# Kernel optimization log

Hardware: AMD Instinct MI355X
Metric: run time of the kernel (lower is better)

Reference implementation:

```python
import jax, jax.numpy as jnp
import numpy as np

NUM_QUERIES, NUM_KEYS = 32, 64
QUERY_DIM, KEY_DIM = 512, 512
NUM_HEADS, ATTN_DIM = 8, 64
EMBED_DIM = NUM_HEADS * ATTN_DIM  # 512
OUT_DIM = 512
TEMPERATURE = float(np.sqrt(ATTN_DIM))


def setup_inputs() -> dict:
    key = jax.random.key(0)
    ks = jax.random.split(key, 6)
    b = 1.0 / TEMPERATURE
    b_p = 1.0 / float(np.sqrt(OUT_DIM))
    q = jax.random.normal(ks[0], (NUM_QUERIES, 2048, QUERY_DIM), dtype=jnp.float32)
    k = jax.random.normal(ks[1], (NUM_KEYS, 2048, KEY_DIM), dtype=jnp.float32)
    query_weight = jax.random.uniform(ks[2], (NUM_QUERIES, QUERY_DIM, EMBED_DIM), minval=-b, maxval=b, dtype=jnp.float32)
    key_weight = jax.random.uniform(ks[3], (NUM_KEYS, KEY_DIM, EMBED_DIM), minval=-b, maxval=b, dtype=jnp.float32)
    value_weight = jax.random.uniform(ks[4], (NUM_KEYS, KEY_DIM, EMBED_DIM), minval=-b, maxval=b, dtype=jnp.float32)
    proj_weight = jax.random.uniform(ks[5], (NUM_QUERIES, EMBED_DIM, OUT_DIM), minval=-b_p, maxval=b_p, dtype=jnp.float32)
    return {"q": q, "k": k, "query_weight": query_weight, "key_weight": key_weight,
            "value_weight": value_weight, "proj_weight": proj_weight}


def reference(q, k, query_weight, key_weight, value_weight, proj_weight):
    Qn, bs, _ = q.shape
    Kn = k.shape[0]
    H, D = NUM_HEADS, ATTN_DIM
    # per-slot projections: (slots, bs, embed) -> split embed into heads
    query = jnp.einsum('ibq,iqe->ibe', q, query_weight).reshape(Qn, bs, H, D)
    key_e = jnp.einsum('jbk,jke->jbe', k, key_weight).reshape(Kn, bs, H, D)
    value = jnp.einsum('jbk,jke->jbe', k, value_weight).reshape(Kn, bs, H, D)
    # logits over key slots per (batch, head, query slot)
    logits = jnp.einsum('ibhd,jbhd->bhij', query, key_e) / TEMPERATURE
    attn = jax.nn.softmax(logits, axis=-1)  # softmax over key slots
    out = jnp.einsum('bhij,jbhd->ibhd', attn, value).reshape(Qn, bs, H * D)
    out = jnp.einsum('ibe,ieo->ibo', out, proj_weight)
    return out
```

## Files before the change

kernel.cpp:

```cpp
#include <hip/hip_runtime.h>

typedef __attribute__((ext_vector_type(8))) short bf16x8;
typedef __attribute__((ext_vector_type(4))) float f32x4;
typedef __attribute__((ext_vector_type(4))) unsigned short us4;

__device__ __forceinline__ unsigned short f2bf(float f) {
    unsigned u = __builtin_bit_cast(unsigned, f);
    u += 0x7FFFu + ((u >> 16) & 1u);
    return (unsigned short)(u >> 16);
}

__device__ __forceinline__ void gl_lds16(const void* g, void* l) {
    __builtin_amdgcn_global_load_lds(
        (const __attribute__((address_space(1))) unsigned int*)g,
        (__attribute__((address_space(3))) unsigned int*)l, 16, 0, 0);
}

__global__ __launch_bounds__(256) void cast_f32_bf16(const float* __restrict__ in,
                                                     unsigned short* __restrict__ out, int n4) {
    int i = blockIdx.x * blockDim.x + threadIdx.x;
    int stride = gridDim.x * blockDim.x;
    for (; i < n4; i += stride) {
        float4 v = ((const float4*)in)[i];
        us4 o;
        o.x = f2bf(v.x); o.y = f2bf(v.y); o.z = f2bf(v.z); o.w = f2bf(v.w);
        ((us4*)out)[i] = o;
    }
}

__global__ __launch_bounds__(256) void transpose_w(const float* __restrict__ wq,
                                                   const float* __restrict__ wk,
                                                   const float* __restrict__ wv,
                                                   const float* __restrict__ wp,
                                                   unsigned short* __restrict__ Wt) {
    int sb = blockIdx.x >> 6;
    int tile = blockIdx.x & 63;
    const float* src;
    if (sb < 32)       src = wq + (size_t)sb * 262144;
    else if (sb < 96)  src = wk + (size_t)(sb - 32) * 262144;
    else if (sb < 160) src = wv + (size_t)(sb - 96) * 262144;
    else               src = wp + (size_t)(sb - 160) * 262144;
    unsigned short* dst = Wt + (size_t)sb * 262144;
    int q0 = (tile & 7) * 64, e0 = (tile >> 3) * 64;
    __shared__ float t[64][65];
    int tx = threadIdx.x & 63, ty = threadIdx.x >> 6;
    for (int i = 0; i < 16; i++) {
        int r = ty + 4 * i;
        t[r][tx] = src[(size_t)(q0 + r) * 512 + e0 + tx];
    }
    __syncthreads();
    int tx2 = threadIdx.x & 31, ty2 = threadIdx.x >> 5;
    for (int i = 0; i < 8; i++) {
        int e = ty2 + 8 * i;
        int qq = tx2 * 2;
        unsigned a = f2bf(t[qq][e]);
        unsigned bb = f2bf(t[qq + 1][e]);
        *(unsigned*)&dst[(size_t)(e0 + e) * 512 + q0 + qq] = a | (bb << 16);
    }
}

__global__ __launch_bounds__(256, 2) void gemm_qkv(const unsigned short* __restrict__ qb,
                                                   const unsigned short* __restrict__ kb,
                                                   const unsigned short* __restrict__ Wt,
                                                   unsigned short* __restrict__ Qs,
                                                   unsigned short* __restrict__ Ks,
                                                   unsigned short* __restrict__ Vs) {
    __shared__ __align__(16) unsigned short lds[2][2][8192];
    int s = blockIdx.y;
    const unsigned short* A;
    unsigned short* Cw;
    if (s < 32)      { A = qb + (size_t)s * 1048576;        Cw = Qs + (size_t)s * 1048576; }
    else if (s < 96) { A = kb + (size_t)(s - 32) * 1048576; Cw = Ks + (size_t)(s - 32) * 1048576; }
    else             { A = kb + (size_t)(s - 96) * 1048576; Cw = Vs + (size_t)(s - 96) * 1048576; }
    const unsigned short* B = Wt + (size_t)s * 262144;
    int tm = blockIdx.x >> 2, tn = blockIdx.x & 3;
    int l = threadIdx.x & 63, w = threadIdx.x >> 6;
    const unsigned short* Ag = A + (size_t)(tm * 128) * 512;
    const unsigned short* Bg = B + (size_t)(tn * 128) * 512;
    int wr = (w >> 1) * 64, wc = (w & 1) * 64;
    int srcs = ((l & 7) ^ (l >> 3)) * 8;

    f32x4 acc[4][4] = {};

#define STAGE(bufi, k0)                                                            \
    for (int p = 0; p < 4; p++) {                                                  \
        int row = w * 32 + p * 8 + (l >> 3);                                       \
        gl_lds16(Ag + (size_t)row * 512 + (k0) + srcs, &lds[bufi][0][(w*32+p*8)*64]); \
        gl_lds16(Bg + (size_t)row * 512 + (k0) + srcs, &lds[bufi][1][(w*32+p*8)*64]); \
    }

    STAGE(0, 0)
    __syncthreads();
    for (int t = 0; t < 8; t++) {
        int cur = t & 1;
        if (t < 7) { STAGE(cur ^ 1, (t + 1) * 64) }
        bf16x8 aF[2][4], bF[2][4];
        for (int kc = 0; kc < 2; kc++) {
            int sp = ((kc * 4 + (l >> 4)) ^ (l & 7)) * 8;
            for (int m = 0; m < 4; m++)
                aF[kc][m] = *(const bf16x8*)&lds[cur][0][(wr + m * 16 + (l & 15)) * 64 + sp];
            for (int n = 0; n < 4; n++)
                bF[kc][n] = *(const bf16x8*)&lds[cur][1][(wc + n * 16 + (l & 15)) * 64 + sp];
        }
        for (int kc = 0; kc < 2; kc++)
            for (int m = 0; m < 4; m++)
                for (int n = 0; n < 4; n++)
                    acc[m][n] = __builtin_amdgcn_mfma_f32_16x16x32_bf16(aF[kc][m], bF[kc][n], acc[m][n], 0, 0, 0);
        __syncthreads();
    }
#undef STAGE

    unsigned short* Cs = &lds[0][0][0];
    for (int m = 0; m < 4; m++)
        for (int n = 0; n < 4; n++)
            for (int r = 0; r < 4; r++)
                Cs[(wr + m * 16 + (l >> 4) * 4 + r) * 136 + wc + n * 16 + (l & 15)] = f2bf(acc[m][n][r]);
    __syncthreads();
    for (int rnd = 0; rnd < 8; rnd++) {
        int row = rnd * 16 + (threadIdx.x >> 4);
        int c8 = (threadIdx.x & 15) * 8;
        bf16x8 v = *(const bf16x8*)&Cs[row * 136 + c8];
        *(bf16x8*)&Cw[(size_t)(tm * 128 + row) * 512 + tn * 128 + c8] = v;
    }
}

__global__ __launch_bounds__(256, 2) void gemm_proj(const unsigned short* __restrict__ Ain,
                                                    const unsigned short* __restrict__ Wt,
                                                    float* __restrict__ out) {
    __shared__ __align__(16) unsigned short lds[2][2][8192];
    int s = blockIdx.y;
    const unsigned short* A = Ain + (size_t)s * 1048576;
    const unsigned short* B = Wt + (size_t)(160 + s) * 262144;
    int tm = blockIdx.x >> 2, tn = blockIdx.x & 3;
    int l = threadIdx.x & 63, w = threadIdx.x >> 6;
    const unsigned short* Ag = A + (size_t)(tm * 128) * 512;
    const unsigned short* Bg = B + (size_t)(tn * 128) * 512;
    int wr = (w >> 1) * 64, wc = (w & 1) * 64;
    int srcs = ((l & 7) ^ (l >> 3)) * 8;

    f32x4 acc[4][4] = {};

#define STAGE(bufi, k0)                                                            \
    for (int p = 0; p < 4; p++) {                                                  \
        int row = w * 32 + p * 8 + (l >> 3);                                       \
        gl_lds16(Ag + (size_t)row * 512 + (k0) + srcs, &lds[bufi][0][(w*32+p*8)*64]); \
        gl_lds16(Bg + (size_t)row * 512 + (k0) + srcs, &lds[bufi][1][(w*32+p*8)*64]); \
    }

    STAGE(0, 0)
    __syncthreads();
    for (int t = 0; t < 8; t++) {
        int cur = t & 1;
        if (t < 7) { STAGE(cur ^ 1, (t + 1) * 64) }
        bf16x8 aF[2][4], bF[2][4];
        for (int kc = 0; kc < 2; kc++) {
            int sp = ((kc * 4 + (l >> 4)) ^ (l & 7)) * 8;
            for (int m = 0; m < 4; m++)
                aF[kc][m] = *(const bf16x8*)&lds[cur][0][(wr + m * 16 + (l & 15)) * 64 + sp];
            for (int n = 0; n < 4; n++)
                bF[kc][n] = *(const bf16x8*)&lds[cur][1][(wc + n * 16 + (l & 15)) * 64 + sp];
        }
        for (int kc = 0; kc < 2; kc++)
            for (int m = 0; m < 4; m++)
                for (int n = 0; n < 4; n++)
                    acc[m][n] = __builtin_amdgcn_mfma_f32_16x16x32_bf16(aF[kc][m], bF[kc][n], acc[m][n], 0, 0, 0);
        __syncthreads();
    }
#undef STAGE

    float* Cf = (float*)&lds[0][0][0];
    for (int pass = 0; pass < 2; pass++) {
        if (wr == pass * 64) {
            for (int m = 0; m < 4; m++)
                for (int n = 0; n < 4; n++)
                    for (int r = 0; r < 4; r++)
                        Cf[(m * 16 + (l >> 4) * 4 + r) * 132 + wc + n * 16 + (l & 15)] = acc[m][n][r];
        }
        __syncthreads();
        for (int rnd = 0; rnd < 8; rnd++) {
            int row = rnd * 8 + (threadIdx.x >> 5);
            int c4 = (threadIdx.x & 31) * 4;
            float4 v = *(const float4*)&Cf[row * 132 + c4];
            *(float4*)&out[(size_t)s * 1048576 + (size_t)(tm * 128 + pass * 64 + row) * 512 + tn * 128 + c4] = v;
        }
        __syncthreads();
    }
}

__global__ __launch_bounds__(256) void attn_k(const unsigned short* __restrict__ Qs,
                                              const unsigned short* __restrict__ Ks,
                                              const unsigned short* __restrict__ Vs,
                                              unsigned short* __restrict__ Aout) {
    __shared__ __align__(16) unsigned short pl[4][32 * 72];
    __shared__ __align__(16) unsigned short vt[4][64 * 88];
    const size_t SL = 1048576;
    int w = threadIdx.x >> 6, l = threadIdx.x & 63;
    int g = blockIdx.x * 4 + w;
    int b = g >> 3, h = g & 7;
    const unsigned short* Qp = Qs + (size_t)b * 512 + h * 64;
    const unsigned short* Kp = Ks + (size_t)b * 512 + h * 64;
    const unsigned short* Vp = Vs + (size_t)b * 512 + h * 64;
    int lr = l & 15, lc = l >> 4;
    unsigned short* vtw = vt[w];

    for (int jr = 0; jr < 64; jr += 8) {
        int j = jr + (l >> 3), d0 = (l & 7) * 8;
        bf16x8 v = *(const bf16x8*)&Vp[(size_t)j * SL + d0];
        for (int e = 0; e < 8; e++) vtw[(d0 + e) * 88 + j] = (unsigned short)v[e];
    }

    bf16x8 aQ[2][2], bK[4][2];
    for (int m = 0; m < 2; m++)
        for (int kc = 0; kc < 2; kc++)
            aQ[m][kc] = *(const bf16x8*)&Qp[(size_t)(m * 16 + lr) * SL + kc * 32 + lc * 8];
    for (int n = 0; n < 4; n++)
        for (int kc = 0; kc < 2; kc++)
            bK[n][kc] = *(const bf16x8*)&Kp[(size_t)(n * 16 + lr) * SL + kc * 32 + lc * 8];

    f32x4 acc[2][4] = {};
    for (int kc = 0; kc < 2; kc++)
        for (int m = 0; m < 2; m++)
            for (int n = 0; n < 4; n++)
                acc[m][n] = __builtin_amdgcn_mfma_f32_16x16x32_bf16(aQ[m][kc], bK[n][kc], acc[m][n], 0, 0, 0);

    const float sc = 0.18033688011112042f;
    for (int m = 0; m < 2; m++) {
        for (int r = 0; r < 4; r++) {
            float v = acc[m][0][r];
            for (int n = 1; n < 4; n++) v = fmaxf(v, acc[m][n][r]);
            for (int sh = 1; sh < 16; sh <<= 1) v = fmaxf(v, __shfl_xor(v, sh));
            float ssum = 0.f;
            for (int n = 0; n < 4; n++) {
                float p = exp2f((acc[m][n][r] - v) * sc);
                acc[m][n][r] = p;
                ssum += p;
            }
            for (int sh = 1; sh < 16; sh <<= 1) ssum += __shfl_xor(ssum, sh);
            float inv = 1.0f / ssum;
            for (int n = 0; n < 4; n++)
                pl[w][(m * 16 + lc * 4 + r) * 72 + n * 16 + lr] = f2bf(acc[m][n][r] * inv);
        }
    }

    bf16x8 aP[2][2], bV[4][2];
    for (int m = 0; m < 2; m++)
        for (int kc = 0; kc < 2; kc++)
            aP[m][kc] = *(const bf16x8*)&pl[w][(m * 16 + lr) * 72 + kc * 32 + lc * 8];
    for (int n = 0; n < 4; n++)
        for (int kc = 0; kc < 2; kc++)
            bV[n][kc] = *(const bf16x8*)&vtw[(n * 16 + lr) * 88 + kc * 32 + lc * 8];

    f32x4 o[2][4] = {};
    for (int kc = 0; kc < 2; kc++)
        for (int m = 0; m < 2; m++)
            for (int n = 0; n < 4; n++)
                o[m][n] = __builtin_amdgcn_mfma_f32_16x16x32_bf16(aP[m][kc], bV[n][kc], o[m][n], 0, 0, 0);

    for (int m = 0; m < 2; m++)
        for (int n = 0; n < 4; n++)
            for (int r = 0; r < 4; r++)
                vtw[(m * 16 + lc * 4 + r) * 88 + n * 16 + lr] = f2bf(o[m][n][r]);
    for (int rnd = 0; rnd < 4; rnd++) {
        int i = rnd * 8 + (l >> 3), d0 = (l & 7) * 8;
        bf16x8 v = *(const bf16x8*)&vtw[i * 88 + d0];
        *(bf16x8*)&Aout[(size_t)i * SL + (size_t)b * 512 + h * 64 + d0] = v;
    }
}

extern "C" void kernel_launch(void* const* d_in, const int* in_sizes, int n_in,
                              void* d_out, int out_size, void* d_ws, size_t ws_size,
                              hipStream_t stream) {
    const float* q  = (const float*)d_in[0];
    const float* k  = (const float*)d_in[1];
    const float* wq = (const float*)d_in[2];
    const float* wk = (const float*)d_in[3];
    const float* wv = (const float*)d_in[4];
    const float* wp = (const float*)d_in[5];

    char* ws = (char*)d_ws;
    unsigned short* qb = (unsigned short*)(ws);
    unsigned short* kb = (unsigned short*)(ws + ((size_t)64 << 20));
    unsigned short* Wt = (unsigned short*)(ws + ((size_t)192 << 20));
    unsigned short* Qs = (unsigned short*)(ws + ((size_t)288 << 20));
    unsigned short* Ks = (unsigned short*)(ws + ((size_t)352 << 20));
    unsigned short* Vs = (unsigned short*)(ws + ((size_t)480 << 20));
    unsigned short* Aout = qb;
    float* out = (float*)d_out;

    hipLaunchKernelGGL(cast_f32_bf16, dim3(2048), dim3(256), 0, stream, q, qb, 32 * 2048 * 512 / 4);
    hipLaunchKernelGGL(cast_f32_bf16, dim3(2048), dim3(256), 0, stream, k, kb, 64 * 2048 * 512 / 4);
    hipLaunchKernelGGL(transpose_w, dim3(192 * 64), dim3(256), 0, stream, wq, wk, wv, wp, Wt);
    hipLaunchKernelGGL(gemm_qkv, dim3(64, 160), dim3(256), 0, stream, qb, kb, Wt, Qs, Ks, Vs);
    hipLaunchKernelGGL(attn_k, dim3(4096), dim3(256), 0, stream, Qs, Ks, Vs, Aout);
    hipLaunchKernelGGL(gemm_proj, dim3(64, 32), dim3(256), 0, stream, Aout, Wt, out);
}
```

Baseline: 613.8 us.

## Deepen GEMM pipeline to four LDS stages with XCD-aware block remapping

Both GEMM kernels move from a double-buffered LDS pipeline to a 4-buffer ring that prefetches three k-tiles ahead. Full __syncthreads are replaced with vmcnt-based partial waits plus raw barriers, and MFMA sections are wrapped in s_setprio. The grid is flattened to 1D and remapped so consecutive blocks on each XCD share A tiles, with K and V projections of the same key slot interleaved for L2 reuse. The 64KB LDS buffer drops occupancy to one block per CU, which the deeper prefetch must make up for.

```diff
diff --git a/kernel.cpp b/kernel.cpp
--- a/kernel.cpp
+++ b/kernel.cpp
@@ -59,21 +59,29 @@
     }
 }
 
-__global__ __launch_bounds__(256, 2) void gemm_qkv(const unsigned short* __restrict__ qb,
+__global__ __launch_bounds__(256, 1) void gemm_qkv(const unsigned short* __restrict__ qb,
                                                    const unsigned short* __restrict__ kb,
                                                    const unsigned short* __restrict__ Wt,
                                                    unsigned short* __restrict__ Qs,
                                                    unsigned short* __restrict__ Ks,
                                                    unsigned short* __restrict__ Vs) {
-    __shared__ __align__(16) unsigned short lds[2][2][8192];
-    int s = blockIdx.y;
+    __shared__ __align__(16) unsigned short lds[4][2][8192];
+    int bid = blockIdx.x;
+    int logical = (bid & 7) * 1280 + (bid >> 3);
+    int sIdx = logical >> 6, x = logical & 63;
+    int tm = x >> 2, tn = x & 3;
     const unsigned short* A;
     unsigned short* Cw;
-    if (s < 32)      { A = qb + (size_t)s * 1048576;        Cw = Qs + (size_t)s * 1048576; }
-    else if (s < 96) { A = kb + (size_t)(s - 32) * 1048576; Cw = Ks + (size_t)(s - 32) * 1048576; }
-    else             { A = kb + (size_t)(s - 96) * 1048576; Cw = Vs + (size_t)(s - 96) * 1048576; }
-    const unsigned short* B = Wt + (size_t)s * 262144;
-    int tm = blockIdx.x >> 2, tn = blockIdx.x & 3;
+    int wslot;
+    if (sIdx < 32) {
+        A = qb + (size_t)sIdx * 1048576; Cw = Qs + (size_t)sIdx * 1048576; wslot = sIdx;
+    } else {
+        int p = sIdx - 32, ks = p >> 1;
+        A = kb + (size_t)ks * 1048576;
+        if (p & 1) { Cw = Vs + (size_t)ks * 1048576; wslot = 96 + ks; }
+        else       { Cw = Ks + (size_t)ks * 1048576; wslot = 32 + ks; }
+    }
+    const unsigned short* B = Wt + (size_t)wslot * 262144;
     int l = threadIdx.x & 63, w = threadIdx.x >> 6;
     const unsigned short* Ag = A + (size_t)(tm * 128) * 512;
     const unsigned short* Bg = B + (size_t)(tn * 128) * 512;
@@ -82,34 +90,44 @@
 
     f32x4 acc[4][4] = {};
 
-#define STAGE(bufi, k0)                                                            \
-    for (int p = 0; p < 4; p++) {                                                  \
-        int row = w * 32 + p * 8 + (l >> 3);                                       \
+#define STAGE(bufi, k0)                                                               \
+    for (int p = 0; p < 4; p++) {                                                     \
+        int row = w * 32 + p * 8 + (l >> 3);                                          \
         gl_lds16(Ag + (size_t)row * 512 + (k0) + srcs, &lds[bufi][0][(w*32+p*8)*64]); \
         gl_lds16(Bg + (size_t)row * 512 + (k0) + srcs, &lds[bufi][1][(w*32+p*8)*64]); \
     }
 
-    STAGE(0, 0)
-    __syncthreads();
+    STAGE(0, 0) STAGE(1, 64) STAGE(2, 128)
+    asm volatile("s_waitcnt vmcnt(16)" ::: "memory");
+    __builtin_amdgcn_s_barrier();
+
+#pragma unroll
     for (int t = 0; t < 8; t++) {
-        int cur = t & 1;
-        if (t < 7) { STAGE(cur ^ 1, (t + 1) * 64) }
+        if (t <= 4) { STAGE((t + 3) & 3, (t + 3) * 64) }
+        const unsigned short* la = &lds[t & 3][0][0];
+        const unsigned short* lb = &lds[t & 3][1][0];
         bf16x8 aF[2][4], bF[2][4];
         for (int kc = 0; kc < 2; kc++) {
             int sp = ((kc * 4 + (l >> 4)) ^ (l & 7)) * 8;
             for (int m = 0; m < 4; m++)
-                aF[kc][m] = *(const bf16x8*)&lds[cur][0][(wr + m * 16 + (l & 15)) * 64 + sp];
-            for (int n = 0; n < 4; n++)
-                bF[kc][n] = *(const bf16x8*)&lds[cur][1][(wc + n * 16 + (l & 15)) * 64 + sp];
-        }
+                aF[kc][m] = *(const bf16x8*)&la[(wr + m * 16 + (l & 15)) * 64 + sp];
+            for (int n = 0; n < 4; n++)
+                bF[kc][n] = *(const bf16x8*)&lb[(wc + n * 16 + (l & 15)) * 64 + sp];
+        }
+        __builtin_amdgcn_s_setprio(1);
         for (int kc = 0; kc < 2; kc++)
             for (int m = 0; m < 4; m++)
                 for (int n = 0; n < 4; n++)
                     acc[m][n] = __builtin_amdgcn_mfma_f32_16x16x32_bf16(aF[kc][m], bF[kc][n], acc[m][n], 0, 0, 0);
-        __syncthreads();
+        __builtin_amdgcn_s_setprio(0);
+        if (t <= 4)      asm volatile("s_waitcnt vmcnt(16)" ::: "memory");
+        else if (t == 5) asm volatile("s_waitcnt vmcnt(8)" ::: "memory");
+        else if (t == 6) asm volatile("s_waitcnt vmcnt(0)" ::: "memory");
+        if (t < 7) __builtin_amdgcn_s_barrier();
     }
 #undef STAGE
 
+    __syncthreads();
     unsigned short* Cs = &lds[0][0][0];
     for (int m = 0; m < 4; m++)
         for (int n = 0; n < 4; n++)
@@ -124,14 +142,16 @@
     }
 }
 
-__global__ __launch_bounds__(256, 2) void gemm_proj(const unsigned short* __restrict__ Ain,
+__global__ __launch_bounds__(256, 1) void gemm_proj(const unsigned short* __restrict__ Ain,
                                                     const unsigned short* __restrict__ Wt,
                                                     float* __restrict__ out) {
-    __shared__ __align__(16) unsigned short lds[2][2][8192];
-    int s = blockIdx.y;
+    __shared__ __align__(16) unsigned short lds[4][2][8192];
+    int bid = blockIdx.x;
+    int logical = (bid & 7) * 256 + (bid >> 3);
+    int s = logical >> 6, x = logical & 63;
+    int tm = x >> 2, tn = x & 3;
     const unsigned short* A = Ain + (size_t)s * 1048576;
     const unsigned short* B = Wt + (size_t)(160 + s) * 262144;
-    int tm = blockIdx.x >> 2, tn = blockIdx.x & 3;
     int l = threadIdx.x & 63, w = threadIdx.x >> 6;
     const unsigned short* Ag = A + (size_t)(tm * 128) * 512;
     const unsigned short* Bg = B + (size_t)(tn * 128) * 512;
@@ -140,34 +160,44 @@
 
     f32x4 acc[4][4] = {};
 
-#define STAGE(bufi, k0)                                                            \
-    for (int p = 0; p < 4; p++) {                                                  \
-        int row = w * 32 + p * 8 + (l >> 3);                                       \
+#define STAGE(bufi, k0)                                                               \
+    for (int p = 0; p < 4; p++) {                                                     \
+        int row = w * 32 + p * 8 + (l >> 3);                                          \
         gl_lds16(Ag + (size_t)row * 512 + (k0) + srcs, &lds[bufi][0][(w*32+p*8)*64]); \
         gl_lds16(Bg + (size_t)row * 512 + (k0) + srcs, &lds[bufi][1][(w*32+p*8)*64]); \
     }
 
-    STAGE(0, 0)
-    __syncthreads();
+    STAGE(0, 0) STAGE(1, 64) STAGE(2, 128)
+    asm volatile("s_waitcnt vmcnt(16)" ::: "memory");
+    __builtin_amdgcn_s_barrier();
+
+#pragma unroll
     for (int t = 0; t < 8; t++) {
-        int cur = t & 1;
-        if (t < 7) { STAGE(cur ^ 1, (t + 1) * 64) }
+        if (t <= 4) { STAGE((t + 3) & 3, (t + 3) * 64) }
+        const unsigned short* la = &lds[t & 3][0][0];
+        const unsigned short* lb = &lds[t & 3][1][0];
         bf16x8 aF[2][4], bF[2][4];
         for (int kc = 0; kc < 2; kc++) {
             int sp = ((kc * 4 + (l >> 4)) ^ (l & 7)) * 8;
             for (int m = 0; m < 4; m++)
-                aF[kc][m] = *(const bf16x8*)&lds[cur][0][(wr + m * 16 + (l & 15)) * 64 + sp];
-            for (int n = 0; n < 4; n++)
-                bF[kc][n] = *(const bf16x8*)&lds[cur][1][(wc + n * 16 + (l & 15)) * 64 + sp];
-        }
+                aF[kc][m] = *(const bf16x8*)&la[(wr + m * 16 + (l & 15)) * 64 + sp];
+            for (int n = 0; n < 4; n++)
+                bF[kc][n] = *(const bf16x8*)&lb[(wc + n * 16 + (l & 15)) * 64 + sp];
+        }
+        __builtin_amdgcn_s_setprio(1);
         for (int kc = 0; kc < 2; kc++)
             for (int m = 0; m < 4; m++)
                 for (int n = 0; n < 4; n++)
                     acc[m][n] = __builtin_amdgcn_mfma_f32_16x16x32_bf16(aF[kc][m], bF[kc][n], acc[m][n], 0, 0, 0);
-        __syncthreads();
+        __builtin_amdgcn_s_setprio(0);
+        if (t <= 4)      asm volatile("s_waitcnt vmcnt(16)" ::: "memory");
+        else if (t == 5) asm volatile("s_waitcnt vmcnt(8)" ::: "memory");
+        else if (t == 6) asm volatile("s_waitcnt vmcnt(0)" ::: "memory");
+        if (t < 7) __builtin_amdgcn_s_barrier();
     }
 #undef STAGE
 
+    __syncthreads();
     float* Cf = (float*)&lds[0][0][0];
     for (int pass = 0; pass < 2; pass++) {
         if (wr == pass * 64) {
@@ -290,7 +320,7 @@
     hipLaunchKernelGGL(cast_f32_bf16, dim3(2048), dim3(256), 0, stream, q, qb, 32 * 2048 * 512 / 4);
     hipLaunchKernelGGL(cast_f32_bf16, dim3(2048), dim3(256), 0, stream, k, kb, 64 * 2048 * 512 / 4);
     hipLaunchKernelGGL(transpose_w, dim3(192 * 64), dim3(256), 0, stream, wq, wk, wv, wp, Wt);
-    hipLaunchKernelGGL(gemm_qkv, dim3(64, 160), dim3(256), 0, stream, qb, kb, Wt, Qs, Ks, Vs);
+    hipLaunchKernelGGL(gemm_qkv, dim3(10240), dim3(256), 0, stream, qb, kb, Wt, Qs, Ks, Vs);
     hipLaunchKernelGGL(attn_k, dim3(4096), dim3(256), 0, stream, Qs, Ks, Vs, Aout);
-    hipLaunchKernelGGL(gemm_proj, dim3(64, 32), dim3(256), 0, stream, Aout, Wt, out);
-}
+    hipLaunchKernelGGL(gemm_proj, dim3(2048), dim3(256), 0, stream, Aout, Wt, out);
+}
```

After: 655.7 us. 6.8% more time.

## Use 256x256 tiles with 8 waves and ping-pong pipelined GEMM for projections

Applied to the files above, without the earlier changes.

Replaces the 128x128, 4-wave batched GEMMs for the QKV and output projections with a shared 256x256-tile routine run by 512 threads. The routine uses a fine-grained schedule that interleaves global-to-LDS staging with MFMA quarter blocks, separated by explicit barriers and vmcnt waits, and raises wave priority around the MFMAs. Block indices are remapped across XCDs so that K and V tiles sharing the same input slot run close together. The larger tiles cut operand re-reads from global memory and LDS per FLOP, at the cost of one block per CU, more registers and a more complex barrier schedule.

```diff
diff --git a/kernel.cpp b/kernel.cpp
--- a/kernel.cpp
+++ b/kernel.cpp
@@ -59,131 +59,182 @@
     }
 }
 
-__global__ __launch_bounds__(256, 2) void gemm_qkv(const unsigned short* __restrict__ qb,
+__device__ __forceinline__ void gemm256(const unsigned short* __restrict__ Ag,
+                                        const unsigned short* __restrict__ Bg,
+                                        unsigned short (&lds)[2][2][16384],
+                                        f32x4 (&acc)[8][4]) {
+    const int tid = threadIdx.x;
+    const int l = tid & 63, wid = tid >> 6;
+    const int wr = (wid >> 2) * 128, wc = (wid & 3) * 64;
+    const int lr = l & 15, shi = l >> 4;
+    const int srcs = ((l & 7) ^ ((l >> 3) & 7)) * 8;
+    const int grow = l >> 3;
+
+    bf16x8 af[4][2], bf[2][2][2];
+
+#define STG_(which, hh, t) do {                                                     \
+    const unsigned short* gp = (which) ? Bg : Ag;                                   \
+    _Pragma("unroll")                                                               \
+    for (int q = 0; q < 2; q++) {                                                   \
+        int lrow = (hh) * 128 + wid * 16 + q * 8;                                   \
+        gl_lds16(gp + (size_t)(lrow + grow) * 512 + (t) * 64 + srcs,                \
+                 &lds[(t) & 1][which][lrow * 64]);                                  \
+    } } while (0)
+
+#define LDA_(cur, mh) do {                                                          \
+    _Pragma("unroll") for (int m = 0; m < 4; m++)                                   \
+    _Pragma("unroll") for (int ks = 0; ks < 2; ks++)                                \
+        af[m][ks] = *(const bf16x8*)&lds[cur][0]                                    \
+            [(wr + (mh) * 64 + m * 16 + lr) * 64 + ((ks * 4 + shi) ^ (l & 7)) * 8]; \
+    } while (0)
+
+#define LDB_(cur, nh) do {                                                          \
+    _Pragma("unroll") for (int n = 0; n < 2; n++)                                   \
+    _Pragma("unroll") for (int ks = 0; ks < 2; ks++)                                \
+        bf[nh][n][ks] = *(const bf16x8*)&lds[cur][1]                                \
+            [(wc + (nh) * 32 + n * 16 + lr) * 64 + ((ks * 4 + shi) ^ (l & 7)) * 8]; \
+    } while (0)
+
+#define MM_(mh, nh) do {                                                            \
+    __builtin_amdgcn_s_setprio(1);                                                  \
+    _Pragma("unroll") for (int m = 0; m < 4; m++)                                   \
+    _Pragma("unroll") for (int n = 0; n < 2; n++)                                   \
+    _Pragma("unroll") for (int ks = 0; ks < 2; ks++)                                \
+        acc[(mh) * 4 + m][(nh) * 2 + n] = __builtin_amdgcn_mfma_f32_16x16x32_bf16(  \
+            af[m][ks], bf[nh][n][ks], acc[(mh) * 4 + m][(nh) * 2 + n], 0, 0, 0);    \
+    __builtin_amdgcn_s_setprio(0);                                                  \
+    } while (0)
+
+#define FENCE_ asm volatile("" ::: "memory")
+#define BAR_ do { FENCE_; __builtin_amdgcn_s_barrier(); FENCE_; } while (0)
+
+    STG_(0, 0, 0); STG_(0, 1, 0); STG_(1, 0, 0); STG_(1, 1, 0);
+    STG_(1, 0, 1); STG_(1, 1, 1);
+    asm volatile("s_waitcnt vmcnt(4)" ::: "memory");
+    BAR_;
+
+#pragma unroll
+    for (int i = 0; i < 4; i++) {
+        LDA_(0, 0); LDB_(0, 0);
+        STG_(0, 0, 2 * i + 1);
+        BAR_; MM_(0, 0); BAR_;
+        LDB_(0, 1);
+        STG_(0, 1, 2 * i + 1);
+        BAR_; MM_(0, 1); BAR_;
+        LDA_(0, 1);
+        if (i < 3) STG_(1, 0, 2 * i + 2);
+        BAR_; MM_(1, 0); BAR_;
+        if (i < 3) STG_(1, 1, 2 * i + 2);
+        BAR_; MM_(1, 1);
+        if (i < 3) asm volatile("s_waitcnt vmcnt(4)" ::: "memory");
+        else       asm volatile("s_waitcnt vmcnt(0)" ::: "memory");
+        BAR_;
+        LDA_(1, 0); LDB_(1, 0);
+        if (i < 3) STG_(0, 0, 2 * i + 2);
+        BAR_; MM_(0, 0); BAR_;
+        LDB_(1, 1);
+        if (i < 3) STG_(0, 1, 2 * i + 2);
+        BAR_; MM_(0, 1); BAR_;
+        LDA_(1, 1);
+        if (i <= 2) STG_(1, 0, 2 * i + 3);
+        BAR_; MM_(1, 0); BAR_;
+        if (i <= 2) STG_(1, 1, 2 * i + 3);
+        BAR_; MM_(1, 1);
+        if (i < 3) asm volatile("s_waitcnt vmcnt(4)" ::: "memory");
+        else       asm volatile("s_waitcnt vmcnt(0)" ::: "memory");
+        BAR_;
+    }
+#undef STG_
+#undef LDA_
+#undef LDB_
+#undef MM_
+}
+
+__global__ __launch_bounds__(512, 1) void gemm_qkv(const unsigned short* __restrict__ qb,
                                                    const unsigned short* __restrict__ kb,
                                                    const unsigned short* __restrict__ Wt,
                                                    unsigned short* __restrict__ Qs,
                                                    unsigned short* __restrict__ Ks,
                                                    unsigned short* __restrict__ Vs) {
-    __shared__ __align__(16) unsigned short lds[2][2][8192];
-    int s = blockIdx.y;
+    __shared__ __align__(16) unsigned short lds[2][2][16384];
+    int bid = blockIdx.x;
+    int logical = (bid & 7) * 320 + (bid >> 3);
+    int sIdx = logical >> 4, x = logical & 15;
+    int tm = x >> 1, tn = x & 1;
     const unsigned short* A;
     unsigned short* Cw;
-    if (s < 32)      { A = qb + (size_t)s * 1048576;        Cw = Qs + (size_t)s * 1048576; }
-    else if (s < 96) { A = kb + (size_t)(s - 32) * 1048576; Cw = Ks + (size_t)(s - 32) * 1048576; }
-    else             { A = kb + (size_t)(s - 96) * 1048576; Cw = Vs + (size_t)(s - 96) * 1048576; }
-    const unsigned short* B = Wt + (size_t)s * 262144;
-    int tm = blockIdx.x >> 2, tn = blockIdx.x & 3;
-    int l = threadIdx.x & 63, w = threadIdx.x >> 6;
-    const unsigned short* Ag = A + (size_t)(tm * 128) * 512;
-    const unsigned short* Bg = B + (size_t)(tn * 128) * 512;
-    int wr = (w >> 1) * 64, wc = (w & 1) * 64;
-    int srcs = ((l & 7) ^ (l >> 3)) * 8;
-
-    f32x4 acc[4][4] = {};
-
-#define STAGE(bufi, k0)                                                            \
-    for (int p = 0; p < 4; p++) {                                                  \
-        int row = w * 32 + p * 8 + (l >> 3);                                       \
-        gl_lds16(Ag + (size_t)row * 512 + (k0) + srcs, &lds[bufi][0][(w*32+p*8)*64]); \
-        gl_lds16(Bg + (size_t)row * 512 + (k0) + srcs, &lds[bufi][1][(w*32+p*8)*64]); \
-    }
-
-    STAGE(0, 0)
-    __syncthreads();
-    for (int t = 0; t < 8; t++) {
-        int cur = t & 1;
-        if (t < 7) { STAGE(cur ^ 1, (t + 1) * 64) }
-        bf16x8 aF[2][4], bF[2][4];
-        for (int kc = 0; kc < 2; kc++) {
-            int sp = ((kc * 4 + (l >> 4)) ^ (l & 7)) * 8;
-            for (int m = 0; m < 4; m++)
-                aF[kc][m] = *(const bf16x8*)&lds[cur][0][(wr + m * 16 + (l & 15)) * 64 + sp];
-            for (int n = 0; n < 4; n++)
-                bF[kc][n] = *(const bf16x8*)&lds[cur][1][(wc + n * 16 + (l & 15)) * 64 + sp];
-        }
-        for (int kc = 0; kc < 2; kc++)
-            for (int m = 0; m < 4; m++)
+    int wslot;
+    if (sIdx < 32) {
+        A = qb + (size_t)sIdx * 1048576; Cw = Qs + (size_t)sIdx * 1048576; wslot = sIdx;
+    } else {
+        int p = sIdx - 32, ks = p >> 1;
+        A = kb + (size_t)ks * 1048576;
+        if (p & 1) { Cw = Vs + (size_t)ks * 1048576; wslot = 96 + ks; }
+        else       { Cw = Ks + (size_t)ks * 1048576; wslot = 32 + ks; }
+    }
+    const unsigned short* B = Wt + (size_t)wslot * 262144;
+    const unsigned short* Ag = A + (size_t)(tm * 256) * 512;
+    const unsigned short* Bg = B + (size_t)(tn * 256) * 512;
+
+    f32x4 acc[8][4] = {};
+    gemm256(Ag, Bg, lds, acc);
+
+    const int l = threadIdx.x & 63, wid = threadIdx.x >> 6;
+    const int wm = wid >> 2, wc = (wid & 3) * 64;
+    unsigned short* Cs = &lds[0][0][0];
+    for (int pass = 0; pass < 2; pass++) {
+        __syncthreads();
+        if (wm == pass) {
+            for (int m = 0; m < 8; m++)
                 for (int n = 0; n < 4; n++)
-                    acc[m][n] = __builtin_amdgcn_mfma_f32_16x16x32_bf16(aF[kc][m], bF[kc][n], acc[m][n], 0, 0, 0);
+                    for (int r = 0; r < 4; r++)
+                        Cs[(m * 16 + (l >> 4) * 4 + r) * 264 + wc + n * 16 + (l & 15)] = f2bf(acc[m][n][r]);
+        }
         __syncthreads();
-    }
-#undef STAGE
-
-    unsigned short* Cs = &lds[0][0][0];
-    for (int m = 0; m < 4; m++)
-        for (int n = 0; n < 4; n++)
-            for (int r = 0; r < 4; r++)
-                Cs[(wr + m * 16 + (l >> 4) * 4 + r) * 136 + wc + n * 16 + (l & 15)] = f2bf(acc[m][n][r]);
-    __syncthreads();
-    for (int rnd = 0; rnd < 8; rnd++) {
-        int row = rnd * 16 + (threadIdx.x >> 4);
-        int c8 = (threadIdx.x & 15) * 8;
-        bf16x8 v = *(const bf16x8*)&Cs[row * 136 + c8];
-        *(bf16x8*)&Cw[(size_t)(tm * 128 + row) * 512 + tn * 128 + c8] = v;
-    }
-}
-
-__global__ __launch_bounds__(256, 2) void gemm_proj(const unsigned short* __restrict__ Ain,
+        for (int rnd = 0; rnd < 8; rnd++) {
+            int idx = rnd * 512 + threadIdx.x;
+            int row = idx >> 5, c8 = (idx & 31) * 8;
+            bf16x8 v = *(const bf16x8*)&Cs[row * 264 + c8];
+            *(bf16x8*)&Cw[(size_t)(tm * 256 + pass * 128 + row) * 512 + tn * 256 + c8] = v;
+        }
+    }
+}
+
+__global__ __launch_bounds__(512, 1) void gemm_proj(const unsigned short* __restrict__ Ain,
                                                     const unsigned short* __restrict__ Wt,
                                                     float* __restrict__ out) {
-    __shared__ __align__(16) unsigned short lds[2][2][8192];
-    int s = blockIdx.y;
+    __shared__ __align__(16) unsigned short lds[2][2][16384];
+    int bid = blockIdx.x;
+    int logical = (bid & 7) * 64 + (bid >> 3);
+    int s = logical >> 4, x = logical & 15;
+    int tm = x >> 1, tn = x & 1;
     const unsigned short* A = Ain + (size_t)s * 1048576;
     const unsigned short* B = Wt + (size_t)(160 + s) * 262144;
-    int tm = blockIdx.x >> 2, tn = blockIdx.x & 3;
-    int l = threadIdx.x & 63, w = threadIdx.x >> 6;
-    const unsigned short* Ag = A + (size_t)(tm * 128) * 512;
-    const unsigned short* Bg = B + (size_t)(tn * 128) * 512;
-    int wr = (w >> 1) * 64, wc = (w & 1) * 64;
-    int srcs = ((l & 7) ^ (l >> 3)) * 8;
-
-    f32x4 acc[4][4] = {};
-
-#define STAGE(bufi, k0)                                                            \
-    for (int p = 0; p < 4; p++) {                                                  \
-        int row = w * 32 + p * 8 + (l >> 3);                                       \
-        gl_lds16(Ag + (size_t)row * 512 + (k0) + srcs, &lds[bufi][0][(w*32+p*8)*64]); \
-        gl_lds16(Bg + (size_t)row * 512 + (k0) + srcs, &lds[bufi][1][(w*32+p*8)*64]); \
-    }
-
-    STAGE(0, 0)
-    __syncthreads();
-    for (int t = 0; t < 8; t++) {
-        int cur = t & 1;
-        if (t < 7) { STAGE(cur ^ 1, (t + 1) * 64) }
-        bf16x8 aF[2][4], bF[2][4];
-        for (int kc = 0; kc < 2; kc++) {
-            int sp = ((kc * 4 + (l >> 4)) ^ (l & 7)) * 8;
-            for (int m = 0; m < 4; m++)
-                aF[kc][m] = *(const bf16x8*)&lds[cur][0][(wr + m * 16 + (l & 15)) * 64 + sp];
-            for (int n = 0; n < 4; n++)
-                bF[kc][n] = *(const bf16x8*)&lds[cur][1][(wc + n * 16 + (l & 15)) * 64 + sp];
-        }
-        for (int kc = 0; kc < 2; kc++)
-            for (int m = 0; m < 4; m++)
-                for (int n = 0; n < 4; n++)
-                    acc[m][n] = __builtin_amdgcn_mfma_f32_16x16x32_bf16(aF[kc][m], bF[kc][n], acc[m][n], 0, 0, 0);
+    const unsigned short* Ag = A + (size_t)(tm * 256) * 512;
+    const unsigned short* Bg = B + (size_t)(tn * 256) * 512;
+
+    f32x4 acc[8][4] = {};
+    gemm256(Ag, Bg, lds, acc);
+
+    const int l = threadIdx.x & 63, wid = threadIdx.x >> 6;
+    const int wm = wid >> 2, wc = (wid & 3) * 64;
+    float* Cf = (float*)&lds[0][0][0];
+    for (int pass = 0; pass < 4; pass++) {
         __syncthreads();
-    }
-#undef STAGE
-
-    float* Cf = (float*)&lds[0][0][0];
-    for (int pass = 0; pass < 2; pass++) {
-        if (wr == pass * 64) {
-            for (int m = 0; m < 4; m++)
+        if (wm == (pass >> 1)) {
+            int mb = (pass & 1) * 4;
+            for (int mm = 0; mm < 4; mm++)
                 for (int n = 0; n < 4; n++)
                     for (int r = 0; r < 4; r++)
-                        Cf[(m * 16 + (l >> 4) * 4 + r) * 132 + wc + n * 16 + (l & 15)] = acc[m][n][r];
+                        Cf[(mm * 16 + (l >> 4) * 4 + r) * 260 + wc + n * 16 + (l & 15)] = acc[mb + mm][n][r];
         }
         __syncthreads();
         for (int rnd = 0; rnd < 8; rnd++) {
-            int row = rnd * 8 + (threadIdx.x >> 5);
-            int c4 = (threadIdx.x & 31) * 4;
-            float4 v = *(const float4*)&Cf[row * 132 + c4];
-            *(float4*)&out[(size_t)s * 1048576 + (size_t)(tm * 128 + pass * 64 + row) * 512 + tn * 128 + c4] = v;
-        }
-        __syncthreads();
+            int idx = rnd * 512 + threadIdx.x;
+            int row = idx >> 6, c4 = (idx & 63) * 4;
+            float4 v = *(const float4*)&Cf[row * 260 + c4];
+            *(float4*)&out[(size_t)s * 1048576 + (size_t)(tm * 256 + pass * 64 + row) * 512 + tn * 256 + c4] = v;
+        }
     }
 }
 
@@ -290,7 +341,7 @@
     hipLaunchKernelGGL(cast_f32_bf16, dim3(2048), dim3(256), 0, stream, q, qb, 32 * 2048 * 512 / 4);
     hipLaunchKernelGGL(cast_f32_bf16, dim3(2048), dim3(256), 0, stream, k, kb, 64 * 2048 * 512 / 4);
     hipLaunchKernelGGL(transpose_w, dim3(192 * 64), dim3(256), 0, stream, wq, wk, wv, wp, Wt);
-    hipLaunchKernelGGL(gemm_qkv, dim3(64, 160), dim3(256), 0, stream, qb, kb, Wt, Qs, Ks, Vs);
+    hipLaunchKernelGGL(gemm_qkv, dim3(2560), dim3(512), 0, stream, qb, kb, Wt, Qs, Ks, Vs);
     hipLaunchKernelGGL(attn_k, dim3(4096), dim3(256), 0, stream, Qs, Ks, Vs, Aout);
-    hipLaunchKernelGGL(gemm_proj, dim3(64, 32), dim3(256), 0, stream, Aout, Wt, out);
-}
+    hipLaunchKernelGGL(gemm_proj, dim3(512), dim3(512), 0, stream, Aout, Wt, out);
+}
```

Result: faster. 551.7 us (-10.1%).

## Restructure projection GEMMs with 256x128 tiles, triple-buffered K32 pipeline, XCD-aware block mapping

Applied to the files above, without the earlier changes.

Replaces the two duplicated GEMM kernels with a shared body that uses 512-thread blocks computing 256x128 tiles. The K loop now runs in 32-wide steps with a three-stage LDS ring and explicit vmcnt waits, raw barriers and MFMA priority bumps, so global loads overlap compute more deeply. Block IDs are remapped so consecutive blocks on the same XCD share slots, and the K and V projections of one key slot are placed next to each other to reuse the A tile in L2. The cost is more barriers per iteration, heavier register and LDS use, and a multi-pass epilogue.

```diff
diff --git a/kernel.cpp b/kernel.cpp
--- a/kernel.cpp
+++ b/kernel.cpp
@@ -15,6 +15,9 @@
         (const __attribute__((address_space(1))) unsigned int*)g,
         (__attribute__((address_space(3))) unsigned int*)l, 16, 0, 0);
 }
+
+#define FENCE_ asm volatile("" ::: "memory")
+#define BAR_ do { FENCE_; __builtin_amdgcn_s_barrier(); FENCE_; } while (0)
 
 __global__ __launch_bounds__(256) void cast_f32_bf16(const float* __restrict__ in,
                                                      unsigned short* __restrict__ out, int n4) {
@@ -59,131 +62,155 @@
     }
 }
 
-__global__ __launch_bounds__(256, 2) void gemm_qkv(const unsigned short* __restrict__ qb,
+__device__ __forceinline__ void gemm_body(const unsigned short* __restrict__ Ag,
+                                          const unsigned short* __restrict__ Bg,
+                                          unsigned short (&lds)[3][12288],
+                                          f32x4 (&acc)[4][4]) {
+    const int l = threadIdx.x & 63, wid = threadIdx.x >> 6;
+    const int wr = (wid >> 1) * 64, wc = (wid & 1) * 64;
+    const int lr = l & 15, shi = l >> 4;
+    const int rswz = (l >> 1) & 3;
+    const int s32 = ((l & 3) ^ ((l >> 3) & 3)) * 8;
+    const int grow = l >> 2;
+
+    bf16x8 af[2], bf[4];
+
+#define STG3_(bufi, tt) do {                                                              \
+    gl_lds16(Ag + (size_t)(wid * 16 + grow) * 512 + (tt) * 32 + s32,                      \
+             &lds[bufi][(wid * 16) * 32]);                                                \
+    gl_lds16(Ag + (size_t)(128 + wid * 16 + grow) * 512 + (tt) * 32 + s32,                \
+             &lds[bufi][(128 + wid * 16) * 32]);                                          \
+    gl_lds16(Bg + (size_t)(wid * 16 + grow) * 512 + (tt) * 32 + s32,                      \
+             &lds[bufi][8192 + (wid * 16) * 32]);                                         \
+} while (0)
+
+#define LDA2_(cur, mh) do {                                                               \
+    _Pragma("unroll") for (int m_ = 0; m_ < 2; m_++)                                      \
+        af[m_] = *(const bf16x8*)&lds[cur]                                                \
+            [(wr + ((mh) * 2 + m_) * 16 + lr) * 32 + (shi ^ rswz) * 8];                   \
+} while (0)
+
+#define LDB4_(cur) do {                                                                   \
+    _Pragma("unroll") for (int n_ = 0; n_ < 4; n_++)                                      \
+        bf[n_] = *(const bf16x8*)&lds[cur]                                                \
+            [8192 + (wc + n_ * 16 + lr) * 32 + (shi ^ rswz) * 8];                         \
+} while (0)
+
+#define MM8_(mh) do {                                                                     \
+    __builtin_amdgcn_s_setprio(1);                                                        \
+    _Pragma("unroll") for (int m_ = 0; m_ < 2; m_++)                                      \
+    _Pragma("unroll") for (int n_ = 0; n_ < 4; n_++)                                      \
+        acc[(mh) * 2 + m_][n_] = __builtin_amdgcn_mfma_f32_16x16x32_bf16(                 \
+            af[m_], bf[n_], acc[(mh) * 2 + m_][n_], 0, 0, 0);                             \
+    __builtin_amdgcn_s_setprio(0);                                                        \
+} while (0)
+
+    STG3_(0, 0); STG3_(1, 1);
+    asm volatile("s_waitcnt vmcnt(3)" ::: "memory");
+    BAR_;
+
+#pragma unroll
+    for (int t = 0; t < 16; t++) {
+        const int cur = t % 3;
+        if (t + 2 < 16) STG3_((t + 2) % 3, t + 2);
+        LDA2_(cur, 0); LDB4_(cur);
+        BAR_; MM8_(0); BAR_;
+        LDA2_(cur, 1);
+        BAR_; MM8_(1);
+        if (t < 14)       asm volatile("s_waitcnt vmcnt(3)" ::: "memory");
+        else if (t == 14) asm volatile("s_waitcnt vmcnt(0)" ::: "memory");
+        BAR_;
+    }
+#undef STG3_
+#undef LDA2_
+#undef LDB4_
+#undef MM8_
+}
+
+__global__ __launch_bounds__(512, 4) void gemm_qkv(const unsigned short* __restrict__ qb,
                                                    const unsigned short* __restrict__ kb,
                                                    const unsigned short* __restrict__ Wt,
                                                    unsigned short* __restrict__ Qs,
                                                    unsigned short* __restrict__ Ks,
                                                    unsigned short* __restrict__ Vs) {
-    __shared__ __align__(16) unsigned short lds[2][2][8192];
-    int s = blockIdx.y;
+    __shared__ __align__(16) unsigned short lds[3][12288];
+    int bid = blockIdx.x;
+    int logical = (bid & 7) * 640 + (bid >> 3);
+    int sIdx = logical >> 5, x = logical & 31;
+    int tm = x >> 2, tn = x & 3;
     const unsigned short* A;
     unsigned short* Cw;
-    if (s < 32)      { A = qb + (size_t)s * 1048576;        Cw = Qs + (size_t)s * 1048576; }
-    else if (s < 96) { A = kb + (size_t)(s - 32) * 1048576; Cw = Ks + (size_t)(s - 32) * 1048576; }
-    else             { A = kb + (size_t)(s - 96) * 1048576; Cw = Vs + (size_t)(s - 96) * 1048576; }
-    const unsigned short* B = Wt + (size_t)s * 262144;
-    int tm = blockIdx.x >> 2, tn = blockIdx.x & 3;
-    int l = threadIdx.x & 63, w = threadIdx.x >> 6;
-    const unsigned short* Ag = A + (size_t)(tm * 128) * 512;
-    const unsigned short* Bg = B + (size_t)(tn * 128) * 512;
-    int wr = (w >> 1) * 64, wc = (w & 1) * 64;
-    int srcs = ((l & 7) ^ (l >> 3)) * 8;
+    int wslot;
+    if (sIdx < 32) {
+        A = qb + (size_t)sIdx * 1048576; Cw = Qs + (size_t)sIdx * 1048576; wslot = sIdx;
+    } else {
+        int pp = sIdx - 32, ks = pp >> 1;
+        A = kb + (size_t)ks * 1048576;
+        if (pp & 1) { Cw = Vs + (size_t)ks * 1048576; wslot = 96 + ks; }
+        else        { Cw = Ks + (size_t)ks * 1048576; wslot = 32 + ks; }
+    }
+    const unsigned short* Ag = A + (size_t)(tm * 256) * 512;
+    const unsigned short* Bg = Wt + (size_t)wslot * 262144 + (size_t)(tn * 128) * 512;
 
     f32x4 acc[4][4] = {};
-
-#define STAGE(bufi, k0)                                                            \
-    for (int p = 0; p < 4; p++) {                                                  \
-        int row = w * 32 + p * 8 + (l >> 3);                                       \
-        gl_lds16(Ag + (size_t)row * 512 + (k0) + srcs, &lds[bufi][0][(w*32+p*8)*64]); \
-        gl_lds16(Bg + (size_t)row * 512 + (k0) + srcs, &lds[bufi][1][(w*32+p*8)*64]); \
-    }
-
-    STAGE(0, 0)
-    __syncthreads();
-    for (int t = 0; t < 8; t++) {
-        int cur = t & 1;
-        if (t < 7) { STAGE(cur ^ 1, (t + 1) * 64) }
-        bf16x8 aF[2][4], bF[2][4];
-        for (int kc = 0; kc < 2; kc++) {
-            int sp = ((kc * 4 + (l >> 4)) ^ (l & 7)) * 8;
-            for (int m = 0; m < 4; m++)
-                aF[kc][m] = *(const bf16x8*)&lds[cur][0][(wr + m * 16 + (l & 15)) * 64 + sp];
-            for (int n = 0; n < 4; n++)
-                bF[kc][n] = *(const bf16x8*)&lds[cur][1][(wc + n * 16 + (l & 15)) * 64 + sp];
-        }
-        for (int kc = 0; kc < 2; kc++)
-            for (int m = 0; m < 4; m++)
-                for (int n = 0; n < 4; n++)
-                    acc[m][n] = __builtin_amdgcn_mfma_f32_16x16x32_bf16(aF[kc][m], bF[kc][n], acc[m][n], 0, 0, 0);
+    gemm_body(Ag, Bg, lds, acc);
+
+    const int l = threadIdx.x & 63, wid = threadIdx.x >> 6;
+    const int wm = wid >> 1, wn = wid & 1;
+    unsigned short* Cs = &lds[0][0];
+    for (int pass = 0; pass < 2; pass++) {
         __syncthreads();
-    }
-#undef STAGE
-
-    unsigned short* Cs = &lds[0][0][0];
-    for (int m = 0; m < 4; m++)
-        for (int n = 0; n < 4; n++)
-            for (int r = 0; r < 4; r++)
-                Cs[(wr + m * 16 + (l >> 4) * 4 + r) * 136 + wc + n * 16 + (l & 15)] = f2bf(acc[m][n][r]);
-    __syncthreads();
-    for (int rnd = 0; rnd < 8; rnd++) {
-        int row = rnd * 16 + (threadIdx.x >> 4);
-        int c8 = (threadIdx.x & 15) * 8;
-        bf16x8 v = *(const bf16x8*)&Cs[row * 136 + c8];
-        *(bf16x8*)&Cw[(size_t)(tm * 128 + row) * 512 + tn * 128 + c8] = v;
-    }
-}
-
-__global__ __launch_bounds__(256, 2) void gemm_proj(const unsigned short* __restrict__ Ain,
-                                                    const unsigned short* __restrict__ Wt,
-                                                    float* __restrict__ out) {
-    __shared__ __align__(16) unsigned short lds[2][2][8192];
-    int s = blockIdx.y;
-    const unsigned short* A = Ain + (size_t)s * 1048576;
-    const unsigned short* B = Wt + (size_t)(160 + s) * 262144;
-    int tm = blockIdx.x >> 2, tn = blockIdx.x & 3;
-    int l = threadIdx.x & 63, w = threadIdx.x >> 6;
-    const unsigned short* Ag = A + (size_t)(tm * 128) * 512;
-    const unsigned short* Bg = B + (size_t)(tn * 128) * 512;
-    int wr = (w >> 1) * 64, wc = (w & 1) * 64;
-    int srcs = ((l & 7) ^ (l >> 3)) * 8;
-
-    f32x4 acc[4][4] = {};
-
-#define STAGE(bufi, k0)                                                            \
-    for (int p = 0; p < 4; p++) {                                                  \
-        int row = w * 32 + p * 8 + (l >> 3);                                       \
-        gl_lds16(Ag + (size_t)row * 512 + (k0) + srcs, &lds[bufi][0][(w*32+p*8)*64]); \
-        gl_lds16(Bg + (size_t)row * 512 + (k0) + srcs, &lds[bufi][1][(w*32+p*8)*64]); \
-    }
-
-    STAGE(0, 0)
-    __syncthreads();
-    for (int t = 0; t < 8; t++) {
-        int cur = t & 1;
-        if (t < 7) { STAGE(cur ^ 1, (t + 1) * 64) }
-        bf16x8 aF[2][4], bF[2][4];
-        for (int kc = 0; kc < 2; kc++) {
-            int sp = ((kc * 4 + (l >> 4)) ^ (l & 7)) * 8;
-            for (int m = 0; m < 4; m++)
-                aF[kc][m] = *(const bf16x8*)&lds[cur][0][(wr + m * 16 + (l & 15)) * 64 + sp];
-            for (int n = 0; n < 4; n++)
-                bF[kc][n] = *(const bf16x8*)&lds[cur][1][(wc + n * 16 + (l & 15)) * 64 + sp];
-        }
-        for (int kc = 0; kc < 2; kc++)
-            for (int m = 0; m < 4; m++)
-                for (int n = 0; n < 4; n++)
-                    acc[m][n] = __builtin_amdgcn_mfma_f32_16x16x32_bf16(aF[kc][m], bF[kc][n], acc[m][n], 0, 0, 0);
-        __syncthreads();
-    }
-#undef STAGE
-
-    float* Cf = (float*)&lds[0][0][0];
-    for (int pass = 0; pass < 2; pass++) {
-        if (wr == pass * 64) {
+        if ((wm >> 1) == pass) {
             for (int m = 0; m < 4; m++)
                 for (int n = 0; n < 4; n++)
                     for (int r = 0; r < 4; r++)
-                        Cf[(m * 16 + (l >> 4) * 4 + r) * 132 + wc + n * 16 + (l & 15)] = acc[m][n][r];
+                        Cs[((wm & 1) * 64 + m * 16 + (l >> 4) * 4 + r) * 136
+                           + wn * 64 + n * 16 + (l & 15)] = f2bf(acc[m][n][r]);
         }
         __syncthreads();
-        for (int rnd = 0; rnd < 8; rnd++) {
-            int row = rnd * 8 + (threadIdx.x >> 5);
-            int c4 = (threadIdx.x & 31) * 4;
+        for (int rnd = 0; rnd < 4; rnd++) {
+            int idx = rnd * 512 + threadIdx.x;
+            int row = idx >> 4, c8 = (idx & 15) * 8;
+            bf16x8 v = *(const bf16x8*)&Cs[row * 136 + c8];
+            *(bf16x8*)&Cw[(size_t)(tm * 256 + pass * 128 + row) * 512 + tn * 128 + c8] = v;
+        }
+    }
+}
+
+__global__ __launch_bounds__(512, 4) void gemm_proj(const unsigned short* __restrict__ Ain,
+                                                    const unsigned short* __restrict__ Wt,
+                                                    float* __restrict__ out) {
+    __shared__ __align__(16) unsigned short lds[3][12288];
+    int bid = blockIdx.x;
+    int logical = (bid & 7) * 128 + (bid >> 3);
+    int s = logical >> 5, x = logical & 31;
+    int tm = x >> 2, tn = x & 3;
+    const unsigned short* Ag = Ain + (size_t)s * 1048576 + (size_t)(tm * 256) * 512;
+    const unsigned short* Bg = Wt + (size_t)(160 + s) * 262144 + (size_t)(tn * 128) * 512;
+
+    f32x4 acc[4][4] = {};
+    gemm_body(Ag, Bg, lds, acc);
+
+    const int l = threadIdx.x & 63, wid = threadIdx.x >> 6;
+    const int wm = wid >> 1, wn = wid & 1;
+    float* Cf = (float*)&lds[0][0];
+    for (int pass = 0; pass < 4; pass++) {
+        __syncthreads();
+        if (wm == pass) {
+            for (int m = 0; m < 4; m++)
+                for (int n = 0; n < 4; n++)
+                    for (int r = 0; r < 4; r++)
+                        Cf[(m * 16 + (l >> 4) * 4 + r) * 132
+                           + wn * 64 + n * 16 + (l & 15)] = acc[m][n][r];
+        }
+        __syncthreads();
+        for (int rnd = 0; rnd < 4; rnd++) {
+            int idx = rnd * 512 + threadIdx.x;
+            int row = idx >> 5, c4 = (idx & 31) * 4;
             float4 v = *(const float4*)&Cf[row * 132 + c4];
-            *(float4*)&out[(size_t)s * 1048576 + (size_t)(tm * 128 + pass * 64 + row) * 512 + tn * 128 + c4] = v;
-        }
-        __syncthreads();
+            *(float4*)&out[(size_t)s * 1048576
+                           + (size_t)(tm * 256 + pass * 64 + row) * 512 + tn * 128 + c4] = v;
+        }
     }
 }
 
@@ -290,7 +317,7 @@
     hipLaunchKernelGGL(cast_f32_bf16, dim3(2048), dim3(256), 0, stream, q, qb, 32 * 2048 * 512 / 4);
     hipLaunchKernelGGL(cast_f32_bf16, dim3(2048), dim3(256), 0, stream, k, kb, 64 * 2048 * 512 / 4);
     hipLaunchKernelGGL(transpose_w, dim3(192 * 64), dim3(256), 0, stream, wq, wk, wv, wp, Wt);
-    hipLaunchKernelGGL(gemm_qkv, dim3(64, 160), dim3(256), 0, stream, qb, kb, Wt, Qs, Ks, Vs);
+    hipLaunchKernelGGL(gemm_qkv, dim3(5120), dim3(512), 0, stream, qb, kb, Wt, Qs, Ks, Vs);
     hipLaunchKernelGGL(attn_k, dim3(4096), dim3(256), 0, stream, Qs, Ks, Vs, Aout);
-    hipLaunchKernelGGL(gemm_proj, dim3(64, 32), dim3(256), 0, stream, Aout, Wt, out);
-}
+    hipLaunchKernelGGL(gemm_proj, dim3(1024), dim3(512), 0, stream, Aout, Wt, out);
+}
```

Result: faster. 575.3 us (-6.3%).
